# Kernel optimization log

Hardware: AMD Instinct MI355X
Metric: run time of the kernel (lower is better)

Reference implementation:

```python
import jax, jax.numpy as jnp
import numpy as np
from jax import lax
from jax.scipy.special import logsumexp

ALPHA = 0.8   # weight on shape (soft-DTW) term; (1-ALPHA) on temporal term
GAMMA = 0.01  # soft-DTW smoothing
G = 0.05      # exponential time-weighting rate
BIG = 1e8     # finite stand-in for +inf (keeps gradients NaN-free)


def _softdtw(D, gamma):
    """Soft-DTW value R[N,N] for a single [N,N] cost matrix.
    DP over the 2N-1 anti-diagonals, each diagonal vectorized over rows.
    """
    N = D.shape[0]
    idx = jnp.arange(1, N + 1)  # row indices i of interior cells
    # diagonals k-2 and k-1, stored as length-(N+1) vectors indexed by i
    r2 = jnp.full(N + 1, BIG, D.dtype).at[0].set(0.0)  # holds R[0,0]=0
    r1 = jnp.full(N + 1, BIG, D.dtype)

    def step(carry, k):
        r2, r1 = carry
        j = k + 2 - idx                      # column index for each row on diag k
        valid = (j >= 1) & (j <= N)
        d = jnp.where(valid, D[idx - 1, jnp.clip(j - 1, 0, N - 1)], 0.0)
        a = r2[idx - 1]   # R[i-1, j-1]
        b = r1[idx - 1]   # R[i-1, j]
        c = r1[idx]       # R[i,   j-1]
        sm = -gamma * logsumexp(jnp.stack([-a, -b, -c]) / gamma, axis=0)
        new = jnp.concatenate([jnp.full((1,), BIG, D.dtype),
                               jnp.where(valid, d + sm, BIG)])
        return (r1, new), None

    (_, last), _ = lax.scan(step, (r2, r1), jnp.arange(2 * N - 1))
    return last[N]  # R[N, N]


def _weighted_cost(input, target):
    """Exp-time-weighted pairwise squared-Euclidean cost, [B, N, N]."""
    N = input.shape[1]
    # D[b,i,j] = ||target[b,i] - input[b,j]||^2
    D = jnp.sum((target[:, :, None, :] - input[:, None, :, :]) ** 2, axis=-1)
    w = jnp.exp(G * jnp.arange(N, dtype=D.dtype))
    w = w * (N / jnp.sum(w))  # normalize to mean 1
    return D * w[None, :, None]


def setup_inputs() -> dict:
    key = jax.random.key(0)
    k1, k2 = jax.random.split(key)
    inp = jax.random.normal(k1, (64, 512, 1), dtype=jnp.float32)
    tgt = jax.random.normal(k2, (64, 512, 1), dtype=jnp.float32)
    return {"input": inp, "target": tgt}


def reference(input, target):
    B, N, _ = input.shape
    Dw = _weighted_cost(input, target)  # [B, N, N]
    # shape term: mean soft-DTW value
    loss_shape = jnp.mean(jax.vmap(lambda d: _softdtw(d, GAMMA))(Dw))
    # temporal term: soft alignment path E = dR/dD, penalized by time distortion
    path = jax.vmap(jax.grad(lambda d: _softdtw(d, GAMMA)))(Dw)  # [B, N, N]
    t = jnp.arange(1, N + 1, dtype=Dw.dtype)
    Omega = (t[:, None] - t[None, :]) ** 2  # squared time offsets
    loss_temporal = jnp.mean(jnp.sum(path * Omega, axis=(1, 2))) / (N * N)
    return ALPHA * loss_shape + (1.0 - ALPHA) * loss_temporal
```

## Files before the change

kernel.cpp:

```cpp
#include <hip/hip_runtime.h>
#include <cstddef>
#include <cstdint>

namespace {

constexpr int   kN = 512;
constexpr int   kB = 64;
constexpr float kAlpha = 0.8f;
constexpr float kBig  = 1e8f;
constexpr float kKexp = 144.26950408889634f;
constexpr float kGLn2 = 0.006931471805599453f;
constexpr float kWexp = 0.07213475204444817f;

constexpr int W     = 8;
constexpr int DELTA = 16;
constexpr int LAM   = 80;
constexpr int SMAX  = 574;
constexpr int NSUP  = 71;
constexpr int BUFE  = 592;

__device__ __forceinline__ float dpp_oldshr1(float oldv, float src) {
    const int oi = __builtin_bit_cast(int, oldv);
    const int si = __builtin_bit_cast(int, src);
    const int r  = __builtin_amdgcn_update_dpp(oi, si, 0x138, 0xF, 0xF, false);
    return __builtin_bit_cast(float, r);
}

__global__ __launch_bounds__(512, 2)
void dilate_jvp8(const float* __restrict__ input,
                 const float* __restrict__ target,
                 float* __restrict__ partials,
                 int b0)
{
    __shared__ float  sx[kN + 16];
    __shared__ float2 buf[W + 1][BUFE];
    __shared__ float  sred[W];

    const int tid = (int)threadIdx.x;
    const int w = tid >> 6, u = tid & 63;
    const bool topw = (w == 0);
    const int b = b0 + (int)blockIdx.x;
    const int sOff = w * LAM;

    sx[tid] = input[(size_t)b * kN + tid];
    if (tid < 16) sx[kN + tid] = 0.0f;
    for (int i = tid; i < BUFE; i += 512) buf[0][i] = make_float2(kBig, 0.0f);
    const float tk = target[(size_t)b * kN + tid];

    float ew = exp2f(kWexp * (float)tid);
    float es = ew;
    #pragma unroll
    for (int off = 32; off; off >>= 1) es += __shfl_xor(es, off);
    if (u == 0) sred[w] = es;
    __syncthreads();
    float tot = 0.0f;
    #pragma unroll
    for (int q = 0; q < W; ++q) tot += sred[q];
    const float wk = ew * (512.0f / tot);

    float C0 = kBig, C0d = 0.0f;
    float bval = kBig, bvald = 0.0f;
    float aval = (topw && u == 0) ? 0.0f : kBig;
    float avald = 0.0f;
    float xj = sx[0], xjn = sx[(u == 0) ? 1 : 0];
    float fdr = (float)(64 * w + 2 * u);
    const float2* __restrict__ bufP = buf[w];
    float2* __restrict__ bufN = buf[w + 1];

    for (int m = 0; m < NSUP; ++m) {
        const int base = m * DELTA - sOff;
        if (base >= 64 && base <= 496) {
            #pragma unroll
            for (int dg = 0; dg < DELTA; ++dg) {
                const int s = base + dg;
                const float m0 = fminf(bval, fminf(aval, C0));
                const float mk = m0 * kKexp;
                const float eA = exp2f(fmaf(-kKexp, aval, mk));
                const float eB = exp2f(fmaf(-kKexp, bval, mk));
                const float eC = exp2f(fmaf(-kKexp, C0,   mk));
                const float ss = eA + eB + eC;
                const float ri = __builtin_amdgcn_rcpf(ss);
                const float dx = tk - xj;
                const float cur = fmaf(wk * dx, dx,
                                       fmaf(-kGLn2, __log2f(ss), m0));
                const float sd = fmaf(eA, avald, fmaf(eB, bvald, eC * C0d));
                const float curd = fmaf(ri, sd, fdr * fdr);
                C0 = cur; C0d = curd;
                bufN[s - u] = make_float2(cur, curd);
                aval = bval; avald = bvald;
                const float2 rn = bufP[s + 1];
                bval  = dpp_oldshr1(rn.x, cur);
                bvald = dpp_oldshr1(rn.y, curd);
                xj = xjn;
                xjn = sx[s + 2 - u];
                fdr -= 1.0f;
            }
        } else if (base >= -DELTA && base <= SMAX) {
            #pragma unroll
            for (int dg = 0; dg < DELTA; ++dg) {
                const int s = base + dg;
                if (s == -1) {
                    const float2 r0 = bufP[0];
                    bval  = dpp_oldshr1(r0.x, kBig);
                    bvald = dpp_oldshr1(r0.y, 0.0f);
                } else if (s >= 0 && s <= SMAX) {
                    const int c = s - u;
                    const bool valid = (c >= 0) & (c <= 511);
                    const float m0 = fminf(bval, fminf(aval, C0));
                    const float mk = m0 * kKexp;
                    const float eA = exp2f(fmaf(-kKexp, aval, mk));
                    const float eB = exp2f(fmaf(-kKexp, bval, mk));
                    const float eC = exp2f(fmaf(-kKexp, C0,   mk));
                    const float ss = eA + eB + eC;
                    const float ri = __builtin_amdgcn_rcpf(ss);
                    const float dx = tk - xj;
                    float cur = fmaf(wk * dx, dx,
                                     fmaf(-kGLn2, __log2f(ss), m0));
                    const float sd = fmaf(eA, avald, fmaf(eB, bvald, eC * C0d));
                    float curd = fmaf(ri, sd, fdr * fdr);
                    cur  = valid ? cur  : kBig;
                    curd = valid ? curd : 0.0f;
                    C0 = cur; C0d = curd;
                    if (c >= 0) bufN[c] = make_float2(cur, curd);
                    aval = bval; avald = bvald;
                    const float2 rn = bufP[s + 1];
                    bval  = dpp_oldshr1(rn.x, cur);
                    bvald = dpp_oldshr1(rn.y, curd);
                    xj = xjn;
                    int cc = s + 2 - u;
                    cc = cc < 0 ? 0 : (cc > 511 ? 511 : cc);
                    xjn = sx[cc];
                    fdr -= 1.0f;
                }
            }
        }
        __syncthreads();
    }

    if (tid == 511) {
        const float temporal = C0d * (1.0f / (512.0f * 512.0f));
        partials[b] = (kAlpha * C0 + (1.0f - kAlpha) * temporal)
                    * (1.0f / (float)kB);
    }
}

__global__ void dilate_finalize(const float* __restrict__ partials,
                                float* __restrict__ out) {
    float v = partials[threadIdx.x];
    #pragma unroll
    for (int off = 32; off > 0; off >>= 1) v += __shfl_down(v, off);
    if (threadIdx.x == 0) out[0] = v;
}

}

extern "C" void kernel_launch(void* const* d_in, const int* in_sizes, int n_in,
                              void* d_out, int out_size, void* d_ws, size_t ws_size,
                              hipStream_t stream) {
    (void)in_sizes; (void)n_in; (void)out_size; (void)ws_size;
    const float* input  = (const float*)d_in[0];
    const float* target = (const float*)d_in[1];
    float* out      = (float*)d_out;
    float* partials = (float*)d_ws;

    hipLaunchKernelGGL(dilate_jvp8, dim3(kB), dim3(512), 0, stream,
                       input, target, partials, 0);
    hipLaunchKernelGGL(dilate_finalize, dim3(1), dim3(64), 0, stream,
                       partials, out);
}
```

Before: 201.5 us.

## Carry soft-DTW state in scaled log2 domain and halve superstep width

Stores the DP values pre-scaled by -1/(gamma*ln2) so the logsumexp inner step needs only max, subtractions and exp2, with no per-cell multiplies to rescale. The weighting factor is folded into the scale, and the final value is unscaled once at the end. It also halves the wavefront superstep (DELTA 16 to 8, LAM 80 to 72, NSUP 71 to 135), so each step does less work but the kernel issues more barriers. Large scaled magnitudes may cost some float precision.

```diff
diff --git a/kernel.cpp b/kernel.cpp
--- a/kernel.cpp
+++ b/kernel.cpp
@@ -7,16 +7,16 @@
 constexpr int   kN = 512;
 constexpr int   kB = 64;
 constexpr float kAlpha = 0.8f;
-constexpr float kBig  = 1e8f;
 constexpr float kKexp = 144.26950408889634f;
 constexpr float kGLn2 = 0.006931471805599453f;
 constexpr float kWexp = 0.07213475204444817f;
+constexpr float kZBig = -1.4426950408889634e10f;
 
 constexpr int W     = 8;
-constexpr int DELTA = 16;
-constexpr int LAM   = 80;
+constexpr int DELTA = 8;
+constexpr int LAM   = 72;
 constexpr int SMAX  = 574;
-constexpr int NSUP  = 71;
+constexpr int NSUP  = 135;
 constexpr int BUFE  = 592;
 
 __device__ __forceinline__ float dpp_oldshr1(float oldv, float src) {
@@ -44,7 +44,7 @@
 
     sx[tid] = input[(size_t)b * kN + tid];
     if (tid < 16) sx[kN + tid] = 0.0f;
-    for (int i = tid; i < BUFE; i += 512) buf[0][i] = make_float2(kBig, 0.0f);
+    for (int i = tid; i < BUFE; i += 512) buf[0][i] = make_float2(kZBig, 0.0f);
     const float tk = target[(size_t)b * kN + tid];
 
     float ew = exp2f(kWexp * (float)tid);
@@ -56,11 +56,11 @@
     float tot = 0.0f;
     #pragma unroll
     for (int q = 0; q < W; ++q) tot += sred[q];
-    const float wk = ew * (512.0f / tot);
+    const float wkz = ew * (512.0f / tot) * (-kKexp);
 
-    float C0 = kBig, C0d = 0.0f;
-    float bval = kBig, bvald = 0.0f;
-    float aval = (topw && u == 0) ? 0.0f : kBig;
+    float C0 = kZBig, C0d = 0.0f;
+    float bval = kZBig, bvald = 0.0f;
+    float aval = (topw && u == 0) ? 0.0f : kZBig;
     float avald = 0.0f;
     float xj = sx[0], xjn = sx[(u == 0) ? 1 : 0];
     float fdr = (float)(64 * w + 2 * u);
@@ -69,27 +69,25 @@
 
     for (int m = 0; m < NSUP; ++m) {
         const int base = m * DELTA - sOff;
-        if (base >= 64 && base <= 496) {
+        if (base >= 64 && base <= 504) {
             #pragma unroll
             for (int dg = 0; dg < DELTA; ++dg) {
                 const int s = base + dg;
-                const float m0 = fminf(bval, fminf(aval, C0));
-                const float mk = m0 * kKexp;
-                const float eA = exp2f(fmaf(-kKexp, aval, mk));
-                const float eB = exp2f(fmaf(-kKexp, bval, mk));
-                const float eC = exp2f(fmaf(-kKexp, C0,   mk));
+                const float zm = fmaxf(bval, fmaxf(aval, C0));
+                const float eA = exp2f(aval - zm);
+                const float eB = exp2f(bval - zm);
+                const float eC = exp2f(C0   - zm);
                 const float ss = eA + eB + eC;
                 const float ri = __builtin_amdgcn_rcpf(ss);
                 const float dx = tk - xj;
-                const float cur = fmaf(wk * dx, dx,
-                                       fmaf(-kGLn2, __log2f(ss), m0));
+                const float zcur = fmaf(wkz * dx, dx, zm + __log2f(ss));
                 const float sd = fmaf(eA, avald, fmaf(eB, bvald, eC * C0d));
                 const float curd = fmaf(ri, sd, fdr * fdr);
-                C0 = cur; C0d = curd;
-                bufN[s - u] = make_float2(cur, curd);
+                C0 = zcur; C0d = curd;
+                bufN[s - u] = make_float2(zcur, curd);
                 aval = bval; avald = bvald;
                 const float2 rn = bufP[s + 1];
-                bval  = dpp_oldshr1(rn.x, cur);
+                bval  = dpp_oldshr1(rn.x, zcur);
                 bvald = dpp_oldshr1(rn.y, curd);
                 xj = xjn;
                 xjn = sx[s + 2 - u];
@@ -101,30 +99,28 @@
                 const int s = base + dg;
                 if (s == -1) {
                     const float2 r0 = bufP[0];
-                    bval  = dpp_oldshr1(r0.x, kBig);
+                    bval  = dpp_oldshr1(r0.x, kZBig);
                     bvald = dpp_oldshr1(r0.y, 0.0f);
                 } else if (s >= 0 && s <= SMAX) {
                     const int c = s - u;
                     const bool valid = (c >= 0) & (c <= 511);
-                    const float m0 = fminf(bval, fminf(aval, C0));
-                    const float mk = m0 * kKexp;
-                    const float eA = exp2f(fmaf(-kKexp, aval, mk));
-                    const float eB = exp2f(fmaf(-kKexp, bval, mk));
-                    const float eC = exp2f(fmaf(-kKexp, C0,   mk));
+                    const float zm = fmaxf(bval, fmaxf(aval, C0));
+                    const float eA = exp2f(aval - zm);
+                    const float eB = exp2f(bval - zm);
+                    const float eC = exp2f(C0   - zm);
                     const float ss = eA + eB + eC;
                     const float ri = __builtin_amdgcn_rcpf(ss);
                     const float dx = tk - xj;
-                    float cur = fmaf(wk * dx, dx,
-                                     fmaf(-kGLn2, __log2f(ss), m0));
+                    float zcur = fmaf(wkz * dx, dx, zm + __log2f(ss));
                     const float sd = fmaf(eA, avald, fmaf(eB, bvald, eC * C0d));
                     float curd = fmaf(ri, sd, fdr * fdr);
-                    cur  = valid ? cur  : kBig;
+                    zcur = valid ? zcur : kZBig;
                     curd = valid ? curd : 0.0f;
-                    C0 = cur; C0d = curd;
-                    if (c >= 0) bufN[c] = make_float2(cur, curd);
+                    C0 = zcur; C0d = curd;
+                    if (c >= 0) bufN[c] = make_float2(zcur, curd);
                     aval = bval; avald = bvald;
                     const float2 rn = bufP[s + 1];
-                    bval  = dpp_oldshr1(rn.x, cur);
+                    bval  = dpp_oldshr1(rn.x, zcur);
                     bvald = dpp_oldshr1(rn.y, curd);
                     xj = xjn;
                     int cc = s + 2 - u;
@@ -138,8 +134,9 @@
     }
 
     if (tid == 511) {
+        const float rnn = C0 * (-kGLn2);
         const float temporal = C0d * (1.0f / (512.0f * 512.0f));
-        partials[b] = (kAlpha * C0 + (1.0f - kAlpha) * temporal)
+        partials[b] = (kAlpha * rnn + (1.0f - kAlpha) * temporal)
                     * (1.0f / (float)kB);
     }
 }
```

Result: no change. 202.2 us (+0.4%).
